# Performance work log

Hardware: AMD Instinct MI355X
Metric: run time of the kernel (lower is better)

The kernel has to match this reference:

```python
import jax, jax.numpy as jnp
import numpy as np

B, S, D, H = 4, 1024, 1024, 16
DH = D // H  # head dim = 64
PAD = -1e7   # padding_num in source
EPS = 1e-3   # keras LayerNormalization default epsilon


def setup_inputs() -> dict:
    key = jax.random.key(0)
    ks = jax.random.split(key, 8)
    return {
        "queries": jax.random.normal(ks[0], (B, S, D), jnp.float32),
        "keys": jax.random.normal(ks[1], (B, S, D), jnp.float32),
        "values": jax.random.normal(ks[2], (B, S, D), jnp.float32),
        "query_masks": jax.random.randint(ks[3], (B, S), 0, 2, jnp.int32),
        "key_masks": jax.random.randint(ks[4], (B, S), 0, 2, jnp.int32),
        "Wq": jax.random.normal(ks[5], (D, D), jnp.float32) * (D ** -0.5),
        "Wk": jax.random.normal(ks[6], (D, D), jnp.float32) * (D ** -0.5),
        "Wv": jax.random.normal(ks[7], (D, D), jnp.float32) * (D ** -0.5),
        "gamma": jnp.ones((D,), jnp.float32),
        "beta": jnp.zeros((D,), jnp.float32),
    }


def reference(queries, keys, values, query_masks, key_masks, Wq, Wk, Wv, gamma, beta):
    # QKV projections (no bias)
    Q = queries @ Wq  # [B,S,D]
    K = keys @ Wk
    V = values @ Wv
    # split heads: tf.split(axis=2)+concat(axis=0) == head-major layout [H,B,S,DH]
    Qh = Q.reshape(B, S, H, DH).transpose(2, 0, 1, 3)
    Kh = K.reshape(B, S, H, DH).transpose(2, 0, 1, 3)
    Vh = V.reshape(B, S, H, DH).transpose(2, 0, 1, 3)
    # scaled scores; note source scales by head_dim ** 0.5 (d_k of split K)
    scores = jnp.einsum("hbqd,hbkd->hbqk", Qh, Kh) / (DH ** 0.5)
    # additive key mask: positions where key_mask==0 get large negative
    scores = jnp.where(key_masks[None, :, None, :] == 0, PAD, scores)
    attn = jax.nn.softmax(scores, axis=-1)
    # multiplicative query mask AFTER softmax (as in source)
    attn = attn * query_masks[None, :, :, None].astype(jnp.float32)
    out = jnp.einsum("hbqk,hbkd->hbqd", attn, Vh)  # [H,B,S,DH]
    # merge heads back: concat over feature axis in head order
    out = out.transpose(1, 2, 0, 3).reshape(B, S, D)
    # residual + LayerNorm
    res = queries + out
    mean = jnp.mean(res, axis=-1, keepdims=True)
    var = jnp.mean(jnp.square(res - mean), axis=-1, keepdims=True)
    return gamma * (res - mean) * jax.lax.rsqrt(var + EPS) + beta
```

## Files before the change

### kernel.cpp

```cpp
#include <hip/hip_runtime.h>

#define BB   4
#define SS   1024
#define DD   1024
#define HH   16
#define DHH  64
#define LN_EPS  (1e-3f)

typedef unsigned short u16;
typedef __attribute__((ext_vector_type(8))) short bf16x8;
typedef __attribute__((ext_vector_type(4))) float f32x4;

__device__ __forceinline__ u16 f2bf(float f) {
    union { float f; unsigned int u; } v; v.f = f;
    return (u16)((v.u + 0x7FFFu + ((v.u >> 16) & 1u)) >> 16);
}

__device__ __forceinline__ void cp16(void* lds, const void* g) {
    __builtin_amdgcn_global_load_lds(
        (const __attribute__((address_space(1))) unsigned int*)g,
        (__attribute__((address_space(3))) unsigned int*)lds, 16, 0, 0);
}

__global__ __launch_bounds__(256) void convert3(const float* __restrict__ q,
                                                const float* __restrict__ k,
                                                const float* __restrict__ v,
                                                u16* __restrict__ out) {
    const float* src = (blockIdx.y == 0) ? q : (blockIdx.y == 1) ? k : v;
    u16* dst = out + (size_t)blockIdx.y * ((size_t)BB * SS * DD);
    const int N8 = BB * SS * DD / 8;
    for (int i = blockIdx.x * 256 + threadIdx.x; i < N8; i += gridDim.x * 256) {
        const float4 f0 = ((const float4*)src)[i * 2];
        const float4 f1 = ((const float4*)src)[i * 2 + 1];
        union { u16 u[8]; uint4 o; } t;
        t.u[0] = f2bf(f0.x); t.u[1] = f2bf(f0.y);
        t.u[2] = f2bf(f0.z); t.u[3] = f2bf(f0.w);
        t.u[4] = f2bf(f1.x); t.u[5] = f2bf(f1.y);
        t.u[6] = f2bf(f1.z); t.u[7] = f2bf(f1.w);
        ((uint4*)dst)[i] = t.o;
    }
}

__global__ __launch_bounds__(256) void transpose_w(const float* __restrict__ W0,
                                                   const float* __restrict__ W1,
                                                   const float* __restrict__ W2,
                                                   u16* __restrict__ WtA) {
    const float* W = (blockIdx.z == 0) ? W0 : (blockIdx.z == 1) ? W1 : W2;
    u16* Wt = WtA + (size_t)blockIdx.z * DD * DD;
    __shared__ float Ts[64][65];
    const int tid = threadIdx.x;
    const int k0 = blockIdx.y * 64, n0 = blockIdx.x * 64;
    #pragma unroll
    for (int it = 0; it < 4; ++it) {
        const int idx = tid + it * 256;
        const int r = idx >> 4, c4 = (idx & 15) * 4;
        const float4 v = *(const float4*)&W[(size_t)(k0 + r) * DD + n0 + c4];
        Ts[r][c4 + 0] = v.x; Ts[r][c4 + 1] = v.y;
        Ts[r][c4 + 2] = v.z; Ts[r][c4 + 3] = v.w;
    }
    __syncthreads();
    const int n = tid >> 2, kc = (tid & 3) * 16;
    #pragma unroll
    for (int p = 0; p < 8; ++p) {
        const unsigned int lo = f2bf(Ts[kc + p * 2 + 0][n]);
        const unsigned int hi = f2bf(Ts[kc + p * 2 + 1][n]);
        *(unsigned int*)&Wt[(size_t)(n0 + n) * DD + k0 + kc + p * 2] = lo | (hi << 16);
    }
}

__global__ __launch_bounds__(256) void gemm_fused(const u16* __restrict__ Abf,
                                                  const u16* __restrict__ WtA,
                                                  u16* __restrict__ Qbf,
                                                  u16* __restrict__ Kbf,
                                                  u16* __restrict__ Vtb) {
    __shared__ u16 As[128 * 64];
    __shared__ u16 Bs[128 * 64];
    const int z = blockIdx.z;
    const u16* A = Abf + (size_t)z * BB * SS * DD;
    const u16* B = WtA + (size_t)z * DD * DD;
    const int tid  = threadIdx.x;
    const int wave = tid >> 6, lane = tid & 63;
    const int ln = lane & 15, quad = lane >> 4;
    const int mw = (wave & 1) * 64, nw = (wave >> 1) * 64;
    const int m0 = blockIdx.y * 128, n0 = blockIdx.x * 128;

    f32x4 acc[4][4] = {};

    for (int k0 = 0; k0 < DD; k0 += 64) {
        __syncthreads();
        #pragma unroll
        for (int w = 0; w < 4; ++w) {
            const int s = w * 256 + wave * 64 + lane;
            const int r = s >> 3, csrc = (s & 7) ^ (r & 7);
            cp16(&As[(size_t)(w * 256 + wave * 64) * 8],
                 &A[(size_t)(m0 + r) * DD + k0 + csrc * 8]);
            cp16(&Bs[(size_t)(w * 256 + wave * 64) * 8],
                 &B[(size_t)(n0 + r) * DD + k0 + csrc * 8]);
        }
        __syncthreads();

        #pragma unroll
        for (int kk = 0; kk < 2; ++kk) {
            bf16x8 af[4], bfv[4];
            #pragma unroll
            for (int i = 0; i < 4; ++i) {
                const int r = mw + i * 16 + ln;
                af[i] = *(const bf16x8*)&As[((r << 3) + ((kk * 4 + quad) ^ (r & 7))) << 3];
            }
            #pragma unroll
            for (int j = 0; j < 4; ++j) {
                const int r = nw + j * 16 + ln;
                bfv[j] = *(const bf16x8*)&Bs[((r << 3) + ((kk * 4 + quad) ^ (r & 7))) << 3];
            }
            #pragma unroll
            for (int i = 0; i < 4; ++i)
                #pragma unroll
                for (int j = 0; j < 4; ++j)
                    acc[i][j] = __builtin_amdgcn_mfma_f32_16x16x32_bf16(af[i], bfv[j], acc[i][j], 0, 0, 0);
        }
    }

    if (z < 2) {
        u16* C = (z == 0) ? Qbf : Kbf;
        const float scale = (z == 0) ? 0.125f : 1.0f;
        #pragma unroll
        for (int i = 0; i < 4; ++i) {
            const int mbase = m0 + mw + i * 16 + quad * 4;
            const int bb = mbase >> 10, sb = mbase & 1023;
            #pragma unroll
            for (int j = 0; j < 4; ++j) {
                const int n = n0 + nw + j * 16 + ln;
                const int hh = n >> 6, dh = n & 63;
                #pragma unroll
                for (int r = 0; r < 4; ++r)
                    C[(((size_t)bb * HH + hh) * SS + sb + r) * DHH + dh] =
                        f2bf(acc[i][j][r] * scale);
            }
        }
    } else {
        #pragma unroll
        for (int i = 0; i < 4; ++i) {
            const int mbase = m0 + mw + i * 16 + quad * 4;
            const int bb = mbase >> 10, sb = mbase & 1023;
            #pragma unroll
            for (int j = 0; j < 4; ++j) {
                const int n = n0 + nw + j * 16 + ln;
                const int hh = n >> 6, dh = n & 63;
                uint2 pk;
                pk.x = (unsigned int)f2bf(acc[i][j][0]) | ((unsigned int)f2bf(acc[i][j][1]) << 16);
                pk.y = (unsigned int)f2bf(acc[i][j][2]) | ((unsigned int)f2bf(acc[i][j][3]) << 16);
                *(uint2*)&Vtb[(((size_t)bb * HH + hh) * DHH + dh) * SS + sb] = pk;
            }
        }
    }
}

__global__ __launch_bounds__(256) void attn_mfma(const u16* __restrict__ Qg,
                                                 const u16* __restrict__ Kg,
                                                 const u16* __restrict__ Vtg,
                                                 const int* __restrict__ qmask,
                                                 const int* __restrict__ kmask,
                                                 float* __restrict__ O) {
    __shared__ u16 Qs[64 * 64];
    __shared__ u16 Ks[64 * 64];
    __shared__ u16 Vs[64 * 64];
    __shared__ u16 Ps[64 * 72];
    __shared__ int kms[SS];

    const int bi = blockIdx.x;
    const int qt = bi & 15;
    const int h  = (bi >> 4) & 15;
    const int b  = bi >> 8;
    const int q0 = qt * 64;
    const int tid  = threadIdx.x;
    const int wave = tid >> 6, lane = tid & 63;
    const int ln = lane & 15, quad = lane >> 4;
    const size_t bh = (size_t)b * HH + h;

    #pragma unroll
    for (int w = 0; w < 2; ++w) {
        const int s = w * 256 + wave * 64 + lane;
        const int r = s >> 3, csrc = (s & 7) ^ (r & 7);
        cp16(&Qs[(size_t)(w * 256 + wave * 64) * 8],
             &Qg[(bh * SS + q0 + r) * DHH + csrc * 8]);
    }
    cp16(&kms[wave * 256], &kmask[b * SS + wave * 256 + lane * 4]);
    __syncthreads();

    bf16x8 qf[2];
    #pragma unroll
    for (int kk = 0; kk < 2; ++kk) {
        const int r = wave * 16 + ln;
        qf[kk] = *(const bf16x8*)&Qs[((r << 3) + ((kk * 4 + quad) ^ (r & 7))) << 3];
    }

    f32x4 o[4] = {};
    float lsum[4] = {0.f, 0.f, 0.f, 0.f};
    const f32x4 zero = {0.f, 0.f, 0.f, 0.f};

    for (int kt = 0; kt < SS / 64; ++kt) {
        __syncthreads();
        #pragma unroll
        for (int w = 0; w < 2; ++w) {
            const int s = w * 256 + wave * 64 + lane;
            const int r = s >> 3, csrc = (s & 7) ^ (r & 7);
            cp16(&Ks[(size_t)(w * 256 + wave * 64) * 8],
                 &Kg[(bh * SS + kt * 64 + r) * DHH + csrc * 8]);
            cp16(&Vs[(size_t)(w * 256 + wave * 64) * 8],
                 &Vtg[(bh * DHH + r) * SS + kt * 64 + csrc * 8]);
        }
        __syncthreads();

        #pragma unroll
        for (int nt = 0; nt < 4; ++nt) {
            const int kr = nt * 16 + ln;
            const bf16x8 k0f = *(const bf16x8*)&Ks[((kr << 3) + ((0 + quad) ^ (kr & 7))) << 3];
            const bf16x8 k1f = *(const bf16x8*)&Ks[((kr << 3) + ((4 + quad) ^ (kr & 7))) << 3];
            f32x4 sacc = __builtin_amdgcn_mfma_f32_16x16x32_bf16(qf[0], k0f, zero, 0, 0, 0);
            sacc = __builtin_amdgcn_mfma_f32_16x16x32_bf16(qf[1], k1f, sacc, 0, 0, 0);
            const int km = kms[kt * 64 + kr];
            #pragma unroll
            for (int r = 0; r < 4; ++r) {
                const float p = km ? __expf(sacc[r]) : 0.0f;
                lsum[r] += p;
                Ps[(wave * 16 + quad * 4 + r) * 72 + nt * 16 + ln] = f2bf(p);
            }
        }

        #pragma unroll
        for (int kk2 = 0; kk2 < 2; ++kk2) {
            const bf16x8 pf = *(const bf16x8*)&Ps[(wave * 16 + ln) * 72 + kk2 * 32 + quad * 8];
            #pragma unroll
            for (int nt2 = 0; nt2 < 4; ++nt2) {
                const int vr = nt2 * 16 + ln;
                const bf16x8 vf = *(const bf16x8*)&Vs[((vr << 3) + ((kk2 * 4 + quad) ^ (vr & 7))) << 3];
                o[nt2] = __builtin_amdgcn_mfma_f32_16x16x32_bf16(pf, vf, o[nt2], 0, 0, 0);
            }
        }
    }

    #pragma unroll
    for (int r = 0; r < 4; ++r) {
        #pragma unroll
        for (int off = 1; off < 16; off <<= 1)
            lsum[r] += __shfl_xor(lsum[r], off);
        const int q = q0 + wave * 16 + quad * 4 + r;
        const float scale = (float)qmask[b * SS + q] / lsum[r];
        #pragma unroll
        for (int nt2 = 0; nt2 < 4; ++nt2)
            O[((size_t)b * SS + q) * DD + h * DHH + nt2 * 16 + ln] = o[nt2][r] * scale;
    }
}

__global__ __launch_bounds__(256) void ln_kernel(const float* __restrict__ Qin,
                                                 const float* __restrict__ attn,
                                                 const float* __restrict__ gamma,
                                                 const float* __restrict__ beta,
                                                 float* __restrict__ out) {
    const int row = blockIdx.x;
    const int tid = threadIdx.x;
    const int wid = tid >> 6, lane = tid & 63;
    __shared__ float sred[4];

    const float4 qv = ((const float4*)Qin)[(size_t)row * 256 + tid];
    const float4 av = ((const float4*)attn)[(size_t)row * 256 + tid];
    float4 v;
    v.x = qv.x + av.x; v.y = qv.y + av.y;
    v.z = qv.z + av.z; v.w = qv.w + av.w;

    float sum = v.x + v.y + v.z + v.w;
    #pragma unroll
    for (int off = 32; off; off >>= 1) sum += __shfl_down(sum, off);
    if (lane == 0) sred[wid] = sum;
    __syncthreads();
    const float mean = (sred[0] + sred[1] + sred[2] + sred[3]) * (1.0f / DD);
    __syncthreads();

    const float dx = v.x - mean, dy = v.y - mean, dz = v.z - mean, dw = v.w - mean;
    float vs = dx * dx + dy * dy + dz * dz + dw * dw;
    #pragma unroll
    for (int off = 32; off; off >>= 1) vs += __shfl_down(vs, off);
    if (lane == 0) sred[wid] = vs;
    __syncthreads();
    const float var = (sred[0] + sred[1] + sred[2] + sred[3]) * (1.0f / DD);
    const float inv = rsqrtf(var + LN_EPS);

    const float4 g = ((const float4*)gamma)[tid];
    const float4 bt = ((const float4*)beta)[tid];
    float4 ov;
    ov.x = g.x * dx * inv + bt.x; ov.y = g.y * dy * inv + bt.y;
    ov.z = g.z * dz * inv + bt.z; ov.w = g.w * dw * inv + bt.w;
    ((float4*)out)[(size_t)row * 256 + tid] = ov;
}

extern "C" void kernel_launch(void* const* d_in, const int* in_sizes, int n_in,
                              void* d_out, int out_size, void* d_ws, size_t ws_size,
                              hipStream_t stream) {
    const float* queries = (const float*)d_in[0];
    const float* keys    = (const float*)d_in[1];
    const float* values  = (const float*)d_in[2];
    const int*   qmask   = (const int*)d_in[3];
    const int*   kmask   = (const int*)d_in[4];
    const float* Wq      = (const float*)d_in[5];
    const float* Wk      = (const float*)d_in[6];
    const float* Wv      = (const float*)d_in[7];
    const float* gamma   = (const float*)d_in[8];
    const float* beta    = (const float*)d_in[9];
    float* out = (float*)d_out;

    const size_t NTOK = (size_t)BB * SS;
    u16* Abf = (u16*)d_ws;
    float* Ob = (float*)d_ws;
    u16* Qbf = Abf + 3 * NTOK * DD;
    u16* Kbf = Qbf + NTOK * DD;
    u16* Vtb = Kbf + NTOK * DD;
    u16* WtA = Vtb + NTOK * DD;

    convert3<<<dim3(512, 3), 256, 0, stream>>>(queries, keys, values, Abf);
    transpose_w<<<dim3(16, 16, 3), 256, 0, stream>>>(Wq, Wk, Wv, WtA);

    gemm_fused<<<dim3(DD / 128, NTOK / 128, 3), 256, 0, stream>>>(Abf, WtA, Qbf, Kbf, Vtb);

    attn_mfma<<<BB * HH * (SS / 64), 256, 0, stream>>>(Qbf, Kbf, Vtb, qmask, kmask, Ob);

    ln_kernel<<<BB * SS, 256, 0, stream>>>(queries, Ob, gamma, beta, out);
}
```

Baseline: 208.6 us.

## Merge prep kernels, XCD-aware GEMM block mapping, and 128-key attention tiles

Combines the input conversion and weight transpose into one prep launch. Remaps GEMM blocks so blocks on the same XCD share A rows for better L2 reuse. Doubles the attention K/V tile to 128 keys to halve barrier-separated loads, reusing the Q LDS buffer for P and reading key masks from global memory. This raises LDS usage per block, which may reduce occupancy.

```diff
diff --git a/kernel.cpp b/kernel.cpp
--- a/kernel.cpp
+++ b/kernel.cpp
@@ -22,49 +22,51 @@
         (__attribute__((address_space(3))) unsigned int*)lds, 16, 0, 0);
 }
 
-__global__ __launch_bounds__(256) void convert3(const float* __restrict__ q,
-                                                const float* __restrict__ k,
-                                                const float* __restrict__ v,
-                                                u16* __restrict__ out) {
-    const float* src = (blockIdx.y == 0) ? q : (blockIdx.y == 1) ? k : v;
-    u16* dst = out + (size_t)blockIdx.y * ((size_t)BB * SS * DD);
-    const int N8 = BB * SS * DD / 8;
-    for (int i = blockIdx.x * 256 + threadIdx.x; i < N8; i += gridDim.x * 256) {
-        const float4 f0 = ((const float4*)src)[i * 2];
-        const float4 f1 = ((const float4*)src)[i * 2 + 1];
-        union { u16 u[8]; uint4 o; } t;
-        t.u[0] = f2bf(f0.x); t.u[1] = f2bf(f0.y);
-        t.u[2] = f2bf(f0.z); t.u[3] = f2bf(f0.w);
-        t.u[4] = f2bf(f1.x); t.u[5] = f2bf(f1.y);
-        t.u[6] = f2bf(f1.z); t.u[7] = f2bf(f1.w);
-        ((uint4*)dst)[i] = t.o;
-    }
-}
-
-__global__ __launch_bounds__(256) void transpose_w(const float* __restrict__ W0,
-                                                   const float* __restrict__ W1,
-                                                   const float* __restrict__ W2,
-                                                   u16* __restrict__ WtA) {
-    const float* W = (blockIdx.z == 0) ? W0 : (blockIdx.z == 1) ? W1 : W2;
-    u16* Wt = WtA + (size_t)blockIdx.z * DD * DD;
+__global__ __launch_bounds__(256) void prep(const float* __restrict__ q,
+                                            const float* __restrict__ k,
+                                            const float* __restrict__ v,
+                                            const float* __restrict__ Wq,
+                                            const float* __restrict__ Wk,
+                                            const float* __restrict__ Wv,
+                                            u16* __restrict__ Abf,
+                                            u16* __restrict__ WtA) {
     __shared__ float Ts[64][65];
+    const int z = blockIdx.z;
     const int tid = threadIdx.x;
-    const int k0 = blockIdx.y * 64, n0 = blockIdx.x * 64;
-    #pragma unroll
-    for (int it = 0; it < 4; ++it) {
-        const int idx = tid + it * 256;
-        const int r = idx >> 4, c4 = (idx & 15) * 4;
-        const float4 v = *(const float4*)&W[(size_t)(k0 + r) * DD + n0 + c4];
-        Ts[r][c4 + 0] = v.x; Ts[r][c4 + 1] = v.y;
-        Ts[r][c4 + 2] = v.z; Ts[r][c4 + 3] = v.w;
-    }
-    __syncthreads();
-    const int n = tid >> 2, kc = (tid & 3) * 16;
-    #pragma unroll
-    for (int p = 0; p < 8; ++p) {
-        const unsigned int lo = f2bf(Ts[kc + p * 2 + 0][n]);
-        const unsigned int hi = f2bf(Ts[kc + p * 2 + 1][n]);
-        *(unsigned int*)&Wt[(size_t)(n0 + n) * DD + k0 + kc + p * 2] = lo | (hi << 16);
+    if (z < 3) {
+        const float* src = (z == 0) ? q : (z == 1) ? k : v;
+        u16* dst = Abf + (size_t)z * ((size_t)BB * SS * DD);
+        const int N8 = BB * SS * DD / 8;
+        for (int i = blockIdx.x * 256 + tid; i < N8; i += 256 * 256) {
+            const float4 f0 = ((const float4*)src)[i * 2];
+            const float4 f1 = ((const float4*)src)[i * 2 + 1];
+            union { u16 u[8]; uint4 o; } t;
+            t.u[0] = f2bf(f0.x); t.u[1] = f2bf(f0.y);
+            t.u[2] = f2bf(f0.z); t.u[3] = f2bf(f0.w);
+            t.u[4] = f2bf(f1.x); t.u[5] = f2bf(f1.y);
+            t.u[6] = f2bf(f1.z); t.u[7] = f2bf(f1.w);
+            ((uint4*)dst)[i] = t.o;
+        }
+    } else {
+        const float* W = (z == 3) ? Wq : (z == 4) ? Wk : Wv;
+        u16* Wt = WtA + (size_t)(z - 3) * DD * DD;
+        const int k0 = (blockIdx.x >> 4) * 64, n0 = (blockIdx.x & 15) * 64;
+        #pragma unroll
+        for (int it = 0; it < 4; ++it) {
+            const int idx = tid + it * 256;
+            const int r = idx >> 4, c4 = (idx & 15) * 4;
+            const float4 vv = *(const float4*)&W[(size_t)(k0 + r) * DD + n0 + c4];
+            Ts[r][c4 + 0] = vv.x; Ts[r][c4 + 1] = vv.y;
+            Ts[r][c4 + 2] = vv.z; Ts[r][c4 + 3] = vv.w;
+        }
+        __syncthreads();
+        const int n = tid >> 2, kc = (tid & 3) * 16;
+        #pragma unroll
+        for (int p = 0; p < 8; ++p) {
+            const unsigned int lo = f2bf(Ts[kc + p * 2 + 0][n]);
+            const unsigned int hi = f2bf(Ts[kc + p * 2 + 1][n]);
+            *(unsigned int*)&Wt[(size_t)(n0 + n) * DD + k0 + kc + p * 2] = lo | (hi << 16);
+        }
     }
 }
 
@@ -75,14 +77,20 @@
                                                   u16* __restrict__ Vtb) {
     __shared__ u16 As[128 * 64];
     __shared__ u16 Bs[128 * 64];
-    const int z = blockIdx.z;
+    const int bid = blockIdx.x;
+    const int xcd = bid & 7;
+    const int t   = bid >> 3;
+    const int z   = t >> 5;
+    const int rr  = t & 31;
+    const int m0  = (xcd * 4 + (rr & 3)) * 128;
+    const int n0  = (rr >> 2) * 128;
+
     const u16* A = Abf + (size_t)z * BB * SS * DD;
     const u16* B = WtA + (size_t)z * DD * DD;
     const int tid  = threadIdx.x;
     const int wave = tid >> 6, lane = tid & 63;
     const int ln = lane & 15, quad = lane >> 4;
     const int mw = (wave & 1) * 64, nw = (wave >> 1) * 64;
-    const int m0 = blockIdx.y * 128, n0 = blockIdx.x * 128;
 
     f32x4 acc[4][4] = {};
 
@@ -161,11 +169,9 @@
                                                  const int* __restrict__ qmask,
                                                  const int* __restrict__ kmask,
                                                  float* __restrict__ O) {
-    __shared__ u16 Qs[64 * 64];
-    __shared__ u16 Ks[64 * 64];
-    __shared__ u16 Vs[64 * 64];
-    __shared__ u16 Ps[64 * 72];
-    __shared__ int kms[SS];
+    __shared__ u16 QPs[64 * 68];
+    __shared__ u16 Ks[128 * 64];
+    __shared__ u16 Vs[64 * 128];
 
     const int bi = blockIdx.x;
     const int qt = bi & 15;
@@ -181,60 +187,67 @@
     for (int w = 0; w < 2; ++w) {
         const int s = w * 256 + wave * 64 + lane;
         const int r = s >> 3, csrc = (s & 7) ^ (r & 7);
-        cp16(&Qs[(size_t)(w * 256 + wave * 64) * 8],
+        cp16(&QPs[(size_t)(w * 256 + wave * 64) * 8],
              &Qg[(bh * SS + q0 + r) * DHH + csrc * 8]);
     }
-    cp16(&kms[wave * 256], &kmask[b * SS + wave * 256 + lane * 4]);
     __syncthreads();
 
     bf16x8 qf[2];
     #pragma unroll
     for (int kk = 0; kk < 2; ++kk) {
         const int r = wave * 16 + ln;
-        qf[kk] = *(const bf16x8*)&Qs[((r << 3) + ((kk * 4 + quad) ^ (r & 7))) << 3];
+        qf[kk] = *(const bf16x8*)&QPs[((r << 3) + ((kk * 4 + quad) ^ (r & 7))) << 3];
     }
 
     f32x4 o[4] = {};
     float lsum[4] = {0.f, 0.f, 0.f, 0.f};
     const f32x4 zero = {0.f, 0.f, 0.f, 0.f};
 
-    for (int kt = 0; kt < SS / 64; ++kt) {
-        __syncthreads();
-        #pragma unroll
-        for (int w = 0; w < 2; ++w) {
+    for (int kt = 0; kt < SS / 128; ++kt) {
+        __syncthreads();
+        #pragma unroll
+        for (int w = 0; w < 4; ++w) {
             const int s = w * 256 + wave * 64 + lane;
-            const int r = s >> 3, csrc = (s & 7) ^ (r & 7);
+            const int rk = s >> 3, ck = (s & 7) ^ (rk & 7);
             cp16(&Ks[(size_t)(w * 256 + wave * 64) * 8],
-                 &Kg[(bh * SS + kt * 64 + r) * DHH + csrc * 8]);
+                 &Kg[(bh * SS + kt * 128 + rk) * DHH + ck * 8]);
+        }
+        #pragma unroll
+        for (int w = 0; w < 4; ++w) {
+            const int s = w * 256 + wave * 64 + lane;
+            const int rv = s >> 4, cv = (s & 15) ^ (rv & 15);
             cp16(&Vs[(size_t)(w * 256 + wave * 64) * 8],
-                 &Vtg[(bh * DHH + r) * SS + kt * 64 + csrc * 8]);
-        }
-        __syncthreads();
-
-        #pragma unroll
-        for (int nt = 0; nt < 4; ++nt) {
-            const int kr = nt * 16 + ln;
-            const bf16x8 k0f = *(const bf16x8*)&Ks[((kr << 3) + ((0 + quad) ^ (kr & 7))) << 3];
-            const bf16x8 k1f = *(const bf16x8*)&Ks[((kr << 3) + ((4 + quad) ^ (kr & 7))) << 3];
-            f32x4 sacc = __builtin_amdgcn_mfma_f32_16x16x32_bf16(qf[0], k0f, zero, 0, 0, 0);
-            sacc = __builtin_amdgcn_mfma_f32_16x16x32_bf16(qf[1], k1f, sacc, 0, 0, 0);
-            const int km = kms[kt * 64 + kr];
-            #pragma unroll
-            for (int r = 0; r < 4; ++r) {
-                const float p = km ? __expf(sacc[r]) : 0.0f;
-                lsum[r] += p;
-                Ps[(wave * 16 + quad * 4 + r) * 72 + nt * 16 + ln] = f2bf(p);
-            }
-        }
-
-        #pragma unroll
-        for (int kk2 = 0; kk2 < 2; ++kk2) {
-            const bf16x8 pf = *(const bf16x8*)&Ps[(wave * 16 + ln) * 72 + kk2 * 32 + quad * 8];
-            #pragma unroll
-            for (int nt2 = 0; nt2 < 4; ++nt2) {
-                const int vr = nt2 * 16 + ln;
-                const bf16x8 vf = *(const bf16x8*)&Vs[((vr << 3) + ((kk2 * 4 + quad) ^ (vr & 7))) << 3];
-                o[nt2] = __builtin_amdgcn_mfma_f32_16x16x32_bf16(pf, vf, o[nt2], 0, 0, 0);
+                 &Vtg[(bh * DHH + rv) * SS + kt * 128 + cv * 8]);
+        }
+        __syncthreads();
+
+        #pragma unroll
+        for (int hh = 0; hh < 2; ++hh) {
+            #pragma unroll
+            for (int nt = 0; nt < 4; ++nt) {
+                const int krow = hh * 64 + nt * 16 + ln;
+                const bf16x8 k0f = *(const bf16x8*)&Ks[((krow << 3) + ((0 + quad) ^ (krow & 7))) << 3];
+                const bf16x8 k1f = *(const bf16x8*)&Ks[((krow << 3) + ((4 + quad) ^ (krow & 7))) << 3];
+                f32x4 sacc = __builtin_amdgcn_mfma_f32_16x16x32_bf16(qf[0], k0f, zero, 0, 0, 0);
+                sacc = __builtin_amdgcn_mfma_f32_16x16x32_bf16(qf[1], k1f, sacc, 0, 0, 0);
+                const int km = kmask[b * SS + kt * 128 + hh * 64 + nt * 16 + ln];
+                #pragma unroll
+                for (int r = 0; r < 4; ++r) {
+                    const float p = km ? __expf(sacc[r]) : 0.0f;
+                    lsum[r] += p;
+                    QPs[(wave * 16 + quad * 4 + r) * 68 + nt * 16 + ln] = f2bf(p);
+                }
+            }
+            #pragma unroll
+            for (int kk2 = 0; kk2 < 2; ++kk2) {
+                const bf16x8 pf = *(const bf16x8*)&QPs[(wave * 16 + ln) * 68 + kk2 * 32 + quad * 8];
+                #pragma unroll
+                for (int nt2 = 0; nt2 < 4; ++nt2) {
+                    const int vrow = nt2 * 16 + ln;
+                    const int vch  = hh * 8 + kk2 * 4 + quad;
+                    const bf16x8 vf = *(const bf16x8*)&Vs[((vrow << 4) + (vch ^ (vrow & 15))) << 3];
+                    o[nt2] = __builtin_amdgcn_mfma_f32_16x16x32_bf16(pf, vf, o[nt2], 0, 0, 0);
+                }
             }
         }
     }
@@ -316,10 +329,9 @@
     u16* Vtb = Kbf + NTOK * DD;
     u16* WtA = Vtb + NTOK * DD;
 
-    convert3<<<dim3(512, 3), 256, 0, stream>>>(queries, keys, values, Abf);
-    transpose_w<<<dim3(16, 16, 3), 256, 0, stream>>>(Wq, Wk, Wv, WtA);
-
-    gemm_fused<<<dim3(DD / 128, NTOK / 128, 3), 256, 0, stream>>>(Abf, WtA, Qbf, Kbf, Vtb);
+    prep<<<dim3(256, 1, 6), 256, 0, stream>>>(queries, keys, values, Wq, Wk, Wv, Abf, WtA);
+
+    gemm_fused<<<768, 256, 0, stream>>>(Abf, WtA, Qbf, Kbf, Vtb);
 
     attn_mfma<<<BB * HH * (SS / 64), 256, 0, stream>>>(Qbf, Kbf, Vtb, qmask, kmask, Ob);
 
```

Result: slower. 229.7 us (+10.1%).
